# Kernel optimization log

Measured on AMD Instinct MI355X. Metric: run time of the kernel, lower is better.

Reference implementation:

```python
import jax, jax.numpy as jnp
from jax import lax
import numpy as np

# ----- static optical constants (from config) -----
N = 500            # phase mask grid
PX = 1e-6          # pixel pitch [m]
WL = 532e-9        # wavelength [m]
FL = 0.1           # focal length [m]
RI = 1.0           # refractive index
FWHC = 150e-6      # laser beam FWHC
K = 2.0 * np.pi * RI / WL
QE, DARK_MEAN, READ_STD, GAIN, MAX_ADU = 0.9, 0.005, 1.6, 2.0, 65535.0
MAX_VAL = 4.0e9    # Normalize01 max
PHOTONS = 1.0e6    # photons per emitter (max_intensity-style scaling)
R = 15             # psf_keep_radius -> 31x31 crops

_x = np.arange(-N // 2, N // 2) * PX
_X, _Y = np.meshgrid(_x, _x)
INCIDENT = np.exp(-(_X**2 + _Y**2) / (2.0 * FWHC**2)).astype(np.float32)
_C1 = (np.pi / (WL * FL) * (_X**2 + _Y**2)) % (2.0 * np.pi)
B1 = np.exp(-1j * _C1).astype(np.complex64)
# angular-spectrum gamma, directly in unshifted fft order
_F = np.fft.fftfreq(N, d=PX)
_A, _B = np.meshgrid(RI * WL * _F, RI * WL * _F)
GAMMA = np.sqrt(np.maximum(1.0 - _A**2 - _B**2, 0.0)).astype(np.float32)

def _gauss7():
    m = (7 - 1) / 2.0
    y, x = np.ogrid[-m:m + 1, -m:m + 1]
    h = np.exp(-(x * x + y * y) / 2.0)
    h[h < np.finfo(h.dtype).eps * h.max()] = 0
    return h.astype(np.float32)
GAUSS7 = _gauss7()


def setup_inputs() -> dict:
    key = jax.random.key(0)
    k1, k2, k3, k4, k5, k6, k7 = jax.random.split(key, 7)
    B, Ne = 8, 64
    phase_mask = jax.random.uniform(k1, (N, N), jnp.float32, 0.0, 2.0 * np.pi)
    zs = jax.random.uniform(k2, (Ne,), jnp.float32, 0.0, 1e-4)  # defocus depths [m]
    xyz = jax.random.randint(k3, (B, Ne, 2), 0, 170, jnp.int32) + 15  # in [15,184]
    std_u = jax.random.uniform(k4, (1,), jnp.float32)
    eps_dark = jax.random.normal(k5, (B, 1, 198, 198), jnp.float32)
    eps_photon = jax.random.normal(k6, (B, 1, 198, 198), jnp.float32)
    eps_read = jax.random.normal(k7, (B, 1, 198, 198), jnp.float32)
    return {"phase_mask": phase_mask, "zs": zs, "xyz": xyz, "std_u": std_u,
            "eps_dark": eps_dark, "eps_photon": eps_photon, "eps_read": eps_read}


def _forward(phase_mask, zs, xyz, std_u, eps_dark, eps_photon, eps_read):
    Bn, Ne = xyz.shape[0], xyz.shape[1]
    # --- FFT-based PSF generation (angular spectrum propagation) ---
    field = (INCIDENT * jnp.exp(1j * phase_mask) * B1).astype(jnp.complex64)  # [N,N]
    Ef = jnp.fft.fft2(field)                                                  # [N,N]
    H = jnp.exp(1j * ((K * GAMMA)[None] * zs[:, None, None]))                 # [Ne,N,N]
    Eprop = jnp.fft.ifft2(Ef[None] * H)                                       # [Ne,N,N]
    inten = jnp.abs(Eprop) ** 2
    c = N // 2
    psf = inten[:, c - R:c + R + 1, c - R:c + R + 1]                          # [Ne,31,31]
    psf = psf / (jnp.sum(psf, (-2, -1), keepdims=True) + 1e-12) * PHOTONS
    images4D = jnp.broadcast_to(psf[None], (Bn, Ne, 2 * R + 1, 2 * R + 1))
    # --- imgs4dto3d: scatter-add 31x31 patches into 200x200 canvas ---
    offs = jnp.arange(2 * R + 1) - R
    rows = xyz[..., 0][..., None, None] + offs[None, None, :, None]           # [B,Ne,31,1]
    cols = xyz[..., 1][..., None, None] + offs[None, None, None, :]           # [B,Ne,1,31]
    bidx = jnp.arange(Bn)[:, None, None, None]
    canvas = jnp.zeros((Bn, 200, 200), psf.dtype).at[bidx, rows, cols].add(images4D)
    img = canvas[:, None]                                                     # [B,1,200,200]
    # --- BlurLayer: per-draw std gaussian, conv pad=2 -> 198x198 ---
    std = 0.8 + 0.4 * std_u[0]
    s2 = std * std
    kern = (1.0 / (2.0 * jnp.pi * s2)) * GAUSS7 ** (1.0 / s2)
    blurred = lax.conv_general_dilated(img, kern[None, None], (1, 1),
                                       [(2, 2), (2, 2)],
                                       dimension_numbers=("NCHW", "OIHW", "NCHW"))
    # --- NoiseLayer (reparameterized gaussian approximations) ---
    sig = blurred * QE
    dark = DARK_MEAN + eps_dark * jnp.sqrt(jnp.float32(DARK_MEAN))
    total = jnp.maximum(sig + dark, 0.0)
    noisy = total + eps_photon * jnp.sqrt(jnp.maximum(total, 1e-12))
    elec = noisy + eps_read * READ_STD
    adu = jnp.clip(elec * GAIN, 0.0, MAX_ADU)
    # --- Normalize01 ---
    out = jnp.where(adu <= 10.0, 1.0, jnp.minimum(adu, MAX_VAL)) / MAX_VAL
    return out.astype(jnp.float32)


def reference(phase_mask, zs, xyz, std_u, eps_dark, eps_photon, eps_read):
    return _forward(phase_mask, zs, xyz, std_u, eps_dark, eps_photon, eps_read)
```

## Files before the change

### kernel.cpp

```cpp
#include <hip/hip_runtime.h>
#include <math.h>

#define NN 500
#define NE 64
#define BATCH 8
#define RR 15
#define PW 31
#define CAN 200
#define OHW 198
#define TWO_PI_F 6.28318530717958647692f
#define SETUP_N (BATCH * CAN * CAN + NE + 49)

#define BCH 16
#define BKC 64
#define BSTR 72
#define BG_CHUNK (2 * 64 * BSTR)
#define NLD (BG_CHUNK * 2 / 16)
#define ASCALE (1.0f / 64.0f)
#define PART_HALF_F ((size_t)NE * NN * 64)

using f16x8 = __attribute__((ext_vector_type(8))) _Float16;
using f32x4 = __attribute__((ext_vector_type(4))) float;

__device__ __forceinline__ void fast_sincos_red(float theta, float* s, float* c) {
    const float INV2PI = 0.15915494309189535f;
    const float PI2_HI = 6.28318548202514648f;
    const float PI2_LO = -1.7484556e-7f;
    float n = rintf(theta * INV2PI);
    float r = fmaf(n, -PI2_HI, theta);
    r = fmaf(n, -PI2_LO, r);
    *s = __sinf(r);
    *c = __cosf(r);
}

__global__ void k_setup(const float* __restrict__ std_u,
                        float* __restrict__ kgamma,
                        float2* __restrict__ tw,
                        float* __restrict__ kern,
                        float* __restrict__ canvas,
                        float* __restrict__ psf_sums) {
    int idx = blockIdx.x * blockDim.x + threadIdx.x;
    if (idx < NN) {
        double th = 2.0 * M_PI * (double)idx / (double)NN;
        tw[idx] = make_float2((float)cos(th), (float)sin(th));
    }
    if (idx < BATCH * CAN * CAN) canvas[idx] = 0.f;
    if (idx >= BATCH * CAN * CAN && idx < BATCH * CAN * CAN + NE)
        psf_sums[idx - BATCH * CAN * CAN] = 0.f;
    if (idx >= BATCH * CAN * CAN + NE && idx < SETUP_N) {
        int t = idx - (BATCH * CAN * CAN + NE);
        float stdv = 0.8f + 0.4f * std_u[0];
        float s2 = stdv * stdv;
        int a = t / 7 - 3, b = t % 7 - 3;
        float g = (float)exp(-0.5 * (double)(a * a + b * b));
        kern[t] = (1.0f / (2.0f * (float)M_PI * s2)) * powf(g, 1.0f / s2);
    }
    if (idx >= NN * NN) return;
    int i = idx / NN, j = idx % NN;
    double fy = (double)((i < 250) ? i : i - 500) * 2000.0;
    double fx = (double)((j < 250) ? j : j - 500) * 2000.0;
    double a = 5.32e-7 * fx;
    double b = 5.32e-7 * fy;
    double g = 1.0 - a * a - b * b;
    g = (g > 0.0) ? sqrt(g) : 0.0;
    float Kf = (float)(2.0 * M_PI * 1.0 / 5.32e-7);
    kgamma[idx] = Kf * (float)g;
}

__global__ void k_setup_b(_Float16* __restrict__ Bg) {
    int idx = blockIdx.x * blockDim.x + threadIdx.x;
    if (idx >= BCH * 64 * BSTR) return;
    int c = idx / (64 * BSTR);
    int rem = idx % (64 * BSTR);
    int nu = rem / BSTR, j = rem % BSTR;
    float hi = 0.f, lo = 0.f;
    int kap = c * BKC + j;
    if (j < BKC && kap < 2 * NN) {
        int u = kap >> 1, p = kap & 1;
        int ri = nu >> 1, q = nu & 1;
        int r = 235 + ri;
        int m = (u * r) % NN;
        double th = 2.0 * M_PI * (double)m / (double)NN;
        double wre = cos(th), wim = sin(th);
        double val = (q == 0) ? ((p == 0) ? wre : -wim)
                              : ((p == 0) ? wim : wre);
        float x = (float)val;
        _Float16 h = (_Float16)x;
        hi = (float)h;
        lo = x - (float)h;
    }
    size_t base = (size_t)c * BG_CHUNK + (size_t)nu * BSTR + j;
    Bg[base] = (_Float16)hi;
    Bg[base + (size_t)64 * BSTR] = (_Float16)lo;
}

__device__ __forceinline__ void ct_dft_stages(const float2* xs, const float2* tts,
                                              float2* S, int t,
                                              float2* out1, float2* out2, int* kout) {
    if (t < 250) {
        int d = t / 25;
        int b = t % 25;
        float2 st = tts[(25 * d) % NN];
        float wr = 1.f, wi = 0.f;
        float Er = 0.f, Ei = 0.f, Or_ = 0.f, Oi = 0.f;
#pragma unroll
        for (int a = 0; a < 20; a += 2) {
            float2 x0 = xs[25 * a + b];
            Er += x0.x * wr - x0.y * wi;
            Ei += x0.x * wi + x0.y * wr;
            float nr = wr * st.x - wi * st.y;
            float ni = wr * st.y + wi * st.x;
            float2 x1 = xs[25 * (a + 1) + b];
            Or_ += x1.x * nr - x1.y * ni;
            Oi  += x1.x * ni + x1.y * nr;
            wr = nr * st.x - ni * st.y;
            wi = nr * st.y + ni * st.x;
        }
        S[b * 21 + d]      = make_float2(Er + Or_, Ei + Oi);
        S[b * 21 + d + 10] = make_float2(Er - Or_, Ei - Oi);
    }
    __syncthreads();
    if (t < 250) {
        int k = t;
        int d1 = k % 20;
        int d2 = (d1 + 10) % 20;
        float2 s1 = tts[k];
        float wr = 1.f, wi = 0.f;
        float a1r = 0.f, a1i = 0.f, a2r = 0.f, a2i = 0.f;
#pragma unroll
        for (int b = 0; b < 25; ++b) {
            float2 u1 = S[b * 21 + d1];
            float2 u2 = S[b * 21 + d2];
            a1r += u1.x * wr - u1.y * wi;
            a1i += u1.x * wi + u1.y * wr;
            float sgnb = (b & 1) ? -1.f : 1.f;
            float w2r = sgnb * wr, w2i = sgnb * wi;
            a2r += u2.x * w2r - u2.y * w2i;
            a2i += u2.x * w2i + u2.y * w2r;
            float nr = wr * s1.x - wi * s1.y;
            wi = wr * s1.y + wi * s1.x;
            wr = nr;
        }
        *out1 = make_float2(a1r, a1i);
        *out2 = make_float2(a2r, a2i);
        *kout = k;
    }
}

__global__ void k_dft_rows(const float* __restrict__ phase, float2* __restrict__ dst,
                           const float2* __restrict__ tw) {
    __shared__ __align__(16) float2 xs[NN];
    __shared__ float2 tts[NN];
    __shared__ float2 S[25 * 21];
    int line = blockIdx.x;
    int t = threadIdx.x;
    const float INV2SIG = 2.2222222e7f;
    const float C1M = (float)(M_PI / 5.32e-8);
    float y = (float)(line - 250) * 1e-6f;
    float y2 = y * y;
    const float* prow = phase + (size_t)line * NN;
    for (int n = t; n < NN; n += 256) {
        float x = (float)(n - 250) * 1e-6f;
        float r2 = x * x + y2;
        float inc = __expf(-r2 * INV2SIG);
        float c1 = C1M * r2;
        float b1r = __cosf(c1), b1i = -__sinf(c1);
        float ph = prow[n];
        float sp = __sinf(ph), cp = __cosf(ph);
        float ar = inc * cp, ai = inc * sp;
        xs[n] = make_float2(ar * b1r - ai * b1i, ar * b1i + ai * b1r);
        float2 tt = tw[n];
        tts[n] = make_float2(tt.x, -tt.y);
    }
    __syncthreads();
    float2 o1, o2; int k;
    ct_dft_stages(xs, tts, S, t, &o1, &o2, &k);
    if (t < 250) {
        dst[(size_t)k * NN + line] = o1;
        dst[(size_t)(k + 250) * NN + line] = o2;
    }
}

__global__ void k_dft_cols(const float2* __restrict__ src, float2* __restrict__ dst,
                           const float2* __restrict__ tw) {
    __shared__ __align__(16) float2 xs[NN];
    __shared__ float2 tts[NN];
    __shared__ float2 S[25 * 21];
    int line = blockIdx.x;
    const float2* s = src + (size_t)line * NN;
    int t = threadIdx.x;
    for (int n = t; n < NN; n += 256) {
        xs[n] = s[n];
        float2 tt = tw[n];
        tts[n] = make_float2(tt.x, -tt.y);
    }
    __syncthreads();
    float2 o1, o2; int k;
    ct_dft_stages(xs, tts, S, t, &o1, &o2, &k);
    if (t < 250) {
        float2* dp = dst + (size_t)line * NN;
        dp[k] = o1;
        dp[k + 250] = o2;
    }
}

__global__ void __launch_bounds__(256, 4)
k_prop_mfma(const float2* __restrict__ EfT,
            const float* __restrict__ kgamma,
            const float* __restrict__ zs,
            const _Float16* __restrict__ Bg,
            float* __restrict__ part) {
    __shared__ __align__(16) _Float16 Bbuf[2][BG_CHUNK];
    __shared__ __align__(16) float2 eft[256];
    __shared__ __align__(16) float kgs[256];
    int v = blockIdx.x;
    int kh = blockIdx.y;
    int t = threadIdx.x;
    int w = t >> 6;
    int lane = t & 63;
    int lrow = lane & 15;
    int grp = lane >> 4;

    {
        int u = 256 * kh + t;
        if (u < NN) {
            eft[t] = EfT[(size_t)v * NN + u];
            kgs[t] = kgamma[(size_t)v * NN + u];
        } else {
            eft[t] = make_float2(0.f, 0.f);
            kgs[t] = 0.f;
        }
    }
    {
        const float4* srcb = (const float4*)(Bg + (size_t)(8 * kh) * BG_CHUNK);
        float4* dstb = (float4*)&Bbuf[0][0];
        for (int i = t; i < NLD; i += 256) dstb[i] = srcb[i];
    }
    float zv = zs[w * 16 + lrow];
    __syncthreads();

    f32x4 acc[4] = {};

#define MODSPLIT(ex, ey, kgv, i0) do {                                        \
        float s_, c_;                                                         \
        fast_sincos_red((kgv) * zv, &s_, &c_);                                \
        float yr = ((ex) * c_ - (ey) * s_) * ASCALE;                          \
        float yi = ((ex) * s_ + (ey) * c_) * ASCALE;                          \
        _Float16 h0 = (_Float16)yr;                                           \
        ah[i0] = h0; al[i0] = (_Float16)(yr - (float)h0);                     \
        _Float16 h1 = (_Float16)yi;                                           \
        ah[i0 + 1] = h1; al[i0 + 1] = (_Float16)(yi - (float)h1);             \
    } while (0)

    for (int ci = 0; ci < 8; ++ci) {
        float4 stg[5];
        if (ci + 1 < 8) {
            const float4* srcb =
                (const float4*)(Bg + (size_t)(8 * kh + ci + 1) * BG_CHUNK);
#pragma unroll
            for (int k = 0; k < 5; ++k) {
                int i = t + k * 256;
                if (i < NLD) stg[k] = srcb[i];
            }
        }
        const _Float16* Bb = &Bbuf[ci & 1][0];
#pragma unroll
        for (int sl = 0; sl < 2; ++sl) {
            int s_loc = ci * 2 + sl;
            int u0 = s_loc * 16 + grp * 4;
            f16x8 ah, al;
            {
                float4 e01 = *(const float4*)&eft[u0];
                float4 e23 = *(const float4*)&eft[u0 + 2];
                float4 kg4 = *(const float4*)&kgs[u0];
                MODSPLIT(e01.x, e01.y, kg4.x, 0);
                MODSPLIT(e01.z, e01.w, kg4.y, 2);
                MODSPLIT(e23.x, e23.y, kg4.z, 4);
                MODSPLIT(e23.z, e23.w, kg4.w, 6);
            }
            int koff = sl * 32 + grp * 8;
#pragma unroll
            for (int nt = 0; nt < 4; ++nt) {
                int nu = nt * 16 + lrow;
                f16x8 bh = *(const f16x8*)&Bb[nu * BSTR + koff];
                f16x8 bl = *(const f16x8*)&Bb[64 * BSTR + nu * BSTR + koff];
                acc[nt] = __builtin_amdgcn_mfma_f32_16x16x32_f16(ah, bh, acc[nt], 0, 0, 0);
                acc[nt] = __builtin_amdgcn_mfma_f32_16x16x32_f16(al, bh, acc[nt], 0, 0, 0);
                acc[nt] = __builtin_amdgcn_mfma_f32_16x16x32_f16(ah, bl, acc[nt], 0, 0, 0);
            }
        }
        if (ci + 1 < 8) {
            float4* dstb = (float4*)&Bbuf[(ci + 1) & 1][0];
#pragma unroll
            for (int k = 0; k < 5; ++k) {
                int i = t + k * 256;
                if (i < NLD) dstb[i] = stg[k];
            }
        }
        __syncthreads();
    }
#undef MODSPLIT

    float* pf = part + (size_t)kh * PART_HALF_F;
#pragma unroll
    for (int nt = 0; nt < 4; ++nt) {
        int nu = nt * 16 + lrow;
#pragma unroll
        for (int rg = 0; rg < 4; ++rg) {
            int z = w * 16 + grp * 4 + rg;
            pf[((size_t)z * NN + v) * 64 + nu] = acc[nt][rg];
        }
    }
}

__global__ void k_prop_cols(const float* __restrict__ part,
                            float* __restrict__ psf,
                            float* __restrict__ psf_sums) {
    __shared__ __align__(16) float X2[NN][16];
    int rq = blockIdx.x;
    int z  = blockIdx.y;
    int t  = threadIdx.x;
    const float* p0 = part + ((size_t)z * NN) * 64 + rq * 16;
    const float* p1 = p0 + PART_HALF_F;
    for (int i = t; i < NN * 4; i += 256) {
        int v = i >> 2, q4 = i & 3;
        float4 a = *(const float4*)(p0 + (size_t)v * 64 + q4 * 4);
        float4 b = *(const float4*)(p1 + (size_t)v * 64 + q4 * 4);
        *(float4*)&X2[v][q4 * 4] =
            make_float4(a.x + b.x, a.y + b.y, a.z + b.z, a.w + b.w);
    }
    __syncthreads();
    int ril = t >> 5;
    int ri  = rq * 8 + ril;
    int ci  = t & 31;
    float val = 0.f;
    if (ri < PW && ci < PW) {
        int c = 235 + ci;
        float ar = 0.f, ai = 0.f;
        float sr, si;
        {
            float th = (TWO_PI_F / NN) * (float)(c % NN);
            sincosf(th, &si, &sr);
        }
        for (int vb = 0; vb < 4; ++vb) {
            int v0 = vb * 125;
            float wr, wi;
            float th = (TWO_PI_F / NN) * (float)((v0 * c) % NN);
            sincosf(th, &wi, &wr);
            for (int v = v0; v < v0 + 125; ++v) {
                float2 xy = *(const float2*)&X2[v][2 * ril];
                ar += xy.x * wr - xy.y * wi;
                ai += xy.x * wi + xy.y * wr;
                float nwr = wr * sr - wi * si;
                wi = wr * si + wi * sr;
                wr = nwr;
            }
        }
        const float inv = 64.0f / 250000.0f;
        float re = ar * inv, im = ai * inv;
        val = re * re + im * im;
        psf[(size_t)z * (PW * PW) + ri * PW + ci] = val;
    }
#pragma unroll
    for (int m = 1; m < 64; m <<= 1) val += __shfl_xor(val, m);
    if ((t & 63) == 0) atomicAdd(&psf_sums[z], val);
}

__global__ void k_scatter(const float* __restrict__ psf,
                          const float* __restrict__ psf_sums,
                          const int* __restrict__ xyz,
                          float* __restrict__ canvas) {
    int e = blockIdx.x;
    int b = blockIdx.y;
    int r0 = xyz[(b * NE + e) * 2 + 0] - RR;
    int c0 = xyz[(b * NE + e) * 2 + 1] - RR;
    float sc = 1.0e6f / (psf_sums[e] + 1e-12f);
    float* cb = canvas + (size_t)b * (CAN * CAN);
    for (int p = threadIdx.x; p < PW * PW; p += blockDim.x) {
        int i = p / PW, j = p % PW;
        atomicAdd(cb + (r0 + i) * CAN + (c0 + j), psf[e * PW * PW + p] * sc);
    }
}

__global__ void k_final(const float* __restrict__ canvas,
                        const float* __restrict__ kern,
                        const float* __restrict__ eps_dark,
                        const float* __restrict__ eps_photon,
                        const float* __restrict__ eps_read,
                        float* __restrict__ out) {
    __shared__ float kk[49];
    __shared__ float tile[14][40];
    int b = blockIdx.z;
    int tx = threadIdx.x, ty = threadIdx.y;
    int t = ty * 32 + tx;
    int j0 = blockIdx.x * 32, i0 = blockIdx.y * 8;
    if (t < 49) kk[t] = kern[t];
    const float* cb = canvas + (size_t)b * (CAN * CAN);
    for (int p = t; p < 14 * 38; p += 256) {
        int rr = p / 38, cc = p % 38;
        int gi = i0 + rr - 2, gj = j0 + cc - 2;
        tile[rr][cc] = (gi >= 0 && gi < CAN && gj >= 0 && gj < CAN)
                           ? cb[gi * CAN + gj] : 0.f;
    }
    __syncthreads();
    int i = i0 + ty, j = j0 + tx;
    if (i >= OHW || j >= OHW) return;
    float acc = 0.f;
#pragma unroll
    for (int a = 0; a < 7; ++a)
#pragma unroll
        for (int q = 0; q < 7; ++q)
            acc += tile[ty + a][tx + q] * kk[a * 7 + q];
    int idx = b * (OHW * OHW) + i * OHW + j;
    float sig = acc * 0.9f;
    float dark = 0.005f + eps_dark[idx] * sqrtf(0.005f);
    float total = fmaxf(sig + dark, 0.0f);
    float noisy = total + eps_photon[idx] * sqrtf(fmaxf(total, 1e-12f));
    float elec = noisy + eps_read[idx] * 1.6f;
    float adu = fminf(fmaxf(elec * 2.0f, 0.0f), 65535.0f);
    float v = (adu <= 10.0f) ? 1.0f : fminf(adu, 4.0e9f);
    out[idx] = v / 4.0e9f;
}

extern "C" void kernel_launch(void* const* d_in, const int* in_sizes, int n_in,
                              void* d_out, int out_size, void* d_ws, size_t ws_size,
                              hipStream_t stream) {
    const float* phase    = (const float*)d_in[0];
    const float* zs       = (const float*)d_in[1];
    const int*   xyz      = (const int*)d_in[2];
    const float* std_u    = (const float*)d_in[3];
    const float* epsd     = (const float*)d_in[4];
    const float* epsp     = (const float*)d_in[5];
    const float* epsr     = (const float*)d_in[6];
    float* out = (float*)d_out;

    char* ws = (char*)d_ws;
    size_t off = 0;
    auto alloc = [&](size_t bytes) {
        off = (off + 255) & ~(size_t)255;
        size_t o = off; off += bytes; return o;
    };
    float*  kgamma   = (float*) (ws + alloc((size_t)NN * NN * 4));
    float2* tw       = (float2*)(ws + alloc((size_t)NN * 8));
    float2* R1T      = (float2*)(ws + alloc((size_t)NN * NN * 8));
    float2* EfT      = (float2*)(ws + alloc((size_t)NN * NN * 8));
    float*  part     = (float*) (ws + alloc(2 * PART_HALF_F * 4));
    float*  psf      = (float*) (ws + alloc((size_t)NE * PW * PW * 4));
    float*  psf_sums = (float*) (ws + alloc((size_t)NE * 4));
    float*  kern     = (float*) (ws + alloc((size_t)64 * 4));
    float*  canvas   = (float*) (ws + alloc((size_t)BATCH * CAN * CAN * 4));
    _Float16* Bg     = (_Float16*)(ws + alloc((size_t)BCH * BG_CHUNK * 2));
    (void)ws_size; (void)n_in; (void)in_sizes; (void)out_size;

    k_setup<<<(SETUP_N + 255) / 256, 256, 0, stream>>>(
        std_u, kgamma, tw, kern, canvas, psf_sums);
    k_setup_b<<<(BCH * 64 * BSTR + 255) / 256, 256, 0, stream>>>(Bg);
    k_dft_rows<<<NN, 256, 0, stream>>>(phase, R1T, tw);
    k_dft_cols<<<NN, 256, 0, stream>>>(R1T, EfT, tw);
    k_prop_mfma<<<dim3(NN, 2), 256, 0, stream>>>(EfT, kgamma, zs, Bg, part);
    k_prop_cols<<<dim3(4, NE), 256, 0, stream>>>(part, psf, psf_sums);
    k_scatter<<<dim3(NE, BATCH), 256, 0, stream>>>(psf, psf_sums, xyz, canvas);
    k_final<<<dim3((OHW + 31) / 32, (OHW + 7) / 8, BATCH), dim3(32, 8), 0, stream>>>(
        canvas, kern, epsd, epsp, epsr, out);
}
```

Measured before the change: 160.6 us.

## Switch propagation GEMM to 32x32 MFMA with in-block K-split reduction

The two-block K-split of the propagation GEMM is merged into one block per column. The four waves are split into two K-halves by two z-halves, each using 32x32x16 MFMA tiles, and the two halves are reduced through shared memory before a single coalesced float4 store. This removes the second partial buffer, so the column kernel no longer adds two halves. The B-matrix setup kernel is also folded into k_setup, saving one launch. In exchange the grid is halved to 500 blocks, each block does twice the work with less pipelining (a single B buffer plus an extra barrier per chunk), and the launch bound drops occupancy to 3.

Result: slower. 164.2 us (+2.2%).

```diff
diff --git a/kernel.cpp b/kernel.cpp
--- a/kernel.cpp
+++ b/kernel.cpp
@@ -15,12 +15,10 @@
 #define BKC 64
 #define BSTR 72
 #define BG_CHUNK (2 * 64 * BSTR)
-#define NLD (BG_CHUNK * 2 / 16)
 #define ASCALE (1.0f / 64.0f)
-#define PART_HALF_F ((size_t)NE * NN * 64)
 
 using f16x8 = __attribute__((ext_vector_type(8))) _Float16;
-using f32x4 = __attribute__((ext_vector_type(4))) float;
+using f32x16 = __attribute__((ext_vector_type(16))) float;
 
 __device__ __forceinline__ void fast_sincos_red(float theta, float* s, float* c) {
     const float INV2PI = 0.15915494309189535f;
@@ -38,11 +36,36 @@
                         float2* __restrict__ tw,
                         float* __restrict__ kern,
                         float* __restrict__ canvas,
-                        float* __restrict__ psf_sums) {
+                        float* __restrict__ psf_sums,
+                        _Float16* __restrict__ Bg) {
     int idx = blockIdx.x * blockDim.x + threadIdx.x;
     if (idx < NN) {
         double th = 2.0 * M_PI * (double)idx / (double)NN;
         tw[idx] = make_float2((float)cos(th), (float)sin(th));
+    }
+    if (idx < BCH * 64 * BSTR) {
+        int c = idx / (64 * BSTR);
+        int rem = idx % (64 * BSTR);
+        int nu = rem / BSTR, j = rem % BSTR;
+        float hi = 0.f, lo = 0.f;
+        int kap = c * BKC + j;
+        if (j < BKC && kap < 2 * NN) {
+            int u = kap >> 1, p = kap & 1;
+            int ri = nu >> 1, q = nu & 1;
+            int r = 235 + ri;
+            int m = (u * r) % NN;
+            double th = 2.0 * M_PI * (double)m / (double)NN;
+            double wre = cos(th), wim = sin(th);
+            double val = (q == 0) ? ((p == 0) ? wre : -wim)
+                                  : ((p == 0) ? wim : wre);
+            float x = (float)val;
+            _Float16 h = (_Float16)x;
+            hi = (float)h;
+            lo = x - (float)h;
+        }
+        size_t base = (size_t)c * BG_CHUNK + (size_t)nu * BSTR + j;
+        Bg[base] = (_Float16)hi;
+        Bg[base + (size_t)64 * BSTR] = (_Float16)lo;
     }
     if (idx < BATCH * CAN * CAN) canvas[idx] = 0.f;
     if (idx >= BATCH * CAN * CAN && idx < BATCH * CAN * CAN + NE)
@@ -65,33 +88,6 @@
     g = (g > 0.0) ? sqrt(g) : 0.0;
     float Kf = (float)(2.0 * M_PI * 1.0 / 5.32e-7);
     kgamma[idx] = Kf * (float)g;
-}
-
-__global__ void k_setup_b(_Float16* __restrict__ Bg) {
-    int idx = blockIdx.x * blockDim.x + threadIdx.x;
-    if (idx >= BCH * 64 * BSTR) return;
-    int c = idx / (64 * BSTR);
-    int rem = idx % (64 * BSTR);
-    int nu = rem / BSTR, j = rem % BSTR;
-    float hi = 0.f, lo = 0.f;
-    int kap = c * BKC + j;
-    if (j < BKC && kap < 2 * NN) {
-        int u = kap >> 1, p = kap & 1;
-        int ri = nu >> 1, q = nu & 1;
-        int r = 235 + ri;
-        int m = (u * r) % NN;
-        double th = 2.0 * M_PI * (double)m / (double)NN;
-        double wre = cos(th), wim = sin(th);
-        double val = (q == 0) ? ((p == 0) ? wre : -wim)
-                              : ((p == 0) ? wim : wre);
-        float x = (float)val;
-        _Float16 h = (_Float16)x;
-        hi = (float)h;
-        lo = x - (float)h;
-    }
-    size_t base = (size_t)c * BG_CHUNK + (size_t)nu * BSTR + j;
-    Bg[base] = (_Float16)hi;
-    Bg[base + (size_t)64 * BSTR] = (_Float16)lo;
 }
 
 __device__ __forceinline__ void ct_dft_stages(const float2* xs, const float2* tts,
@@ -204,70 +200,77 @@
     }
 }
 
-__global__ void __launch_bounds__(256, 4)
+__global__ void __launch_bounds__(256, 3)
 k_prop_mfma(const float2* __restrict__ EfT,
             const float* __restrict__ kgamma,
             const float* __restrict__ zs,
             const _Float16* __restrict__ Bg,
             float* __restrict__ part) {
-    __shared__ __align__(16) _Float16 Bbuf[2][BG_CHUNK];
-    __shared__ __align__(16) float2 eft[256];
-    __shared__ __align__(16) float kgs[256];
+    __shared__ __align__(16) char smem[2 * BG_CHUNK * 2 + 512 * 8 + 512 * 4];
+    _Float16* Bbuf = (_Float16*)smem;
+    float2*   eft  = (float2*)(smem + 2 * BG_CHUNK * 2);
+    float*    kgs  = (float*)(smem + 2 * BG_CHUNK * 2 + 512 * 8);
+    float*    ctile = (float*)smem;
+
     int v = blockIdx.x;
-    int kh = blockIdx.y;
     int t = threadIdx.x;
     int w = t >> 6;
+    int wh = w >> 1;
+    int mw = w & 1;
     int lane = t & 63;
-    int lrow = lane & 15;
-    int grp = lane >> 4;
-
+    int l31 = lane & 31;
+    int lk = lane >> 5;
+
+    for (int n = t; n < 512; n += 256) {
+        if (n < NN) {
+            float2 e = EfT[(size_t)v * NN + n];
+            eft[n] = make_float2(e.x * ASCALE, e.y * ASCALE);
+            kgs[n] = kgamma[(size_t)v * NN + n];
+        } else {
+            eft[n] = make_float2(0.f, 0.f);
+            kgs[n] = 0.f;
+        }
+    }
     {
-        int u = 256 * kh + t;
-        if (u < NN) {
-            eft[t] = EfT[(size_t)v * NN + u];
-            kgs[t] = kgamma[(size_t)v * NN + u];
-        } else {
-            eft[t] = make_float2(0.f, 0.f);
-            kgs[t] = 0.f;
-        }
-    }
-    {
-        const float4* srcb = (const float4*)(Bg + (size_t)(8 * kh) * BG_CHUNK);
-        float4* dstb = (float4*)&Bbuf[0][0];
-        for (int i = t; i < NLD; i += 256) dstb[i] = srcb[i];
-    }
-    float zv = zs[w * 16 + lrow];
-    __syncthreads();
-
-    f32x4 acc[4] = {};
+        for (int k = 0; k < 9; ++k) {
+            int i = t + k * 256;
+            int whs = i / 1152, off = i % 1152;
+            ((float4*)Bbuf)[i] =
+                ((const float4*)(Bg + (size_t)(8 * whs) * BG_CHUNK))[off];
+        }
+    }
+    float zv = zs[mw * 32 + l31];
+    __syncthreads();
+
+    f32x16 acc[2] = {};
 
 #define MODSPLIT(ex, ey, kgv, i0) do {                                        \
         float s_, c_;                                                         \
         fast_sincos_red((kgv) * zv, &s_, &c_);                                \
-        float yr = ((ex) * c_ - (ey) * s_) * ASCALE;                          \
-        float yi = ((ex) * s_ + (ey) * c_) * ASCALE;                          \
+        float yr = (ex) * c_ - (ey) * s_;                                     \
+        float yi = (ex) * s_ + (ey) * c_;                                     \
         _Float16 h0 = (_Float16)yr;                                           \
         ah[i0] = h0; al[i0] = (_Float16)(yr - (float)h0);                     \
         _Float16 h1 = (_Float16)yi;                                           \
         ah[i0 + 1] = h1; al[i0 + 1] = (_Float16)(yi - (float)h1);             \
     } while (0)
 
+    const _Float16* Bb = Bbuf + wh * BG_CHUNK;
     for (int ci = 0; ci < 8; ++ci) {
-        float4 stg[5];
+        float4 stg[9];
         if (ci + 1 < 8) {
-            const float4* srcb =
-                (const float4*)(Bg + (size_t)(8 * kh + ci + 1) * BG_CHUNK);
-#pragma unroll
-            for (int k = 0; k < 5; ++k) {
+#pragma unroll
+            for (int k = 0; k < 9; ++k) {
                 int i = t + k * 256;
-                if (i < NLD) stg[k] = srcb[i];
-            }
-        }
-        const _Float16* Bb = &Bbuf[ci & 1][0];
-#pragma unroll
-        for (int sl = 0; sl < 2; ++sl) {
-            int s_loc = ci * 2 + sl;
-            int u0 = s_loc * 16 + grp * 4;
+                int whs = i / 1152, off = i % 1152;
+                stg[k] = ((const float4*)(Bg +
+                            (size_t)(8 * whs + ci + 1) * BG_CHUNK))[off];
+            }
+        }
+#pragma unroll
+        for (int sl = 0; sl < 4; ++sl) {
+            int step = ci * 4 + sl;
+            int u0 = wh * 256 + step * 8 + lk * 4;
             f16x8 ah, al;
             {
                 float4 e01 = *(const float4*)&eft[u0];
@@ -278,38 +281,55 @@
                 MODSPLIT(e23.x, e23.y, kg4.z, 4);
                 MODSPLIT(e23.z, e23.w, kg4.w, 6);
             }
-            int koff = sl * 32 + grp * 8;
-#pragma unroll
-            for (int nt = 0; nt < 4; ++nt) {
-                int nu = nt * 16 + lrow;
+            int koff = sl * 16 + lk * 8;
+#pragma unroll
+            for (int nt = 0; nt < 2; ++nt) {
+                int nu = nt * 32 + l31;
                 f16x8 bh = *(const f16x8*)&Bb[nu * BSTR + koff];
                 f16x8 bl = *(const f16x8*)&Bb[64 * BSTR + nu * BSTR + koff];
-                acc[nt] = __builtin_amdgcn_mfma_f32_16x16x32_f16(ah, bh, acc[nt], 0, 0, 0);
-                acc[nt] = __builtin_amdgcn_mfma_f32_16x16x32_f16(al, bh, acc[nt], 0, 0, 0);
-                acc[nt] = __builtin_amdgcn_mfma_f32_16x16x32_f16(ah, bl, acc[nt], 0, 0, 0);
-            }
-        }
+                acc[nt] = __builtin_amdgcn_mfma_f32_32x32x16_f16(ah, bh, acc[nt], 0, 0, 0);
+                acc[nt] = __builtin_amdgcn_mfma_f32_32x32x16_f16(al, bh, acc[nt], 0, 0, 0);
+                acc[nt] = __builtin_amdgcn_mfma_f32_32x32x16_f16(ah, bl, acc[nt], 0, 0, 0);
+            }
+        }
+        __syncthreads();
         if (ci + 1 < 8) {
-            float4* dstb = (float4*)&Bbuf[(ci + 1) & 1][0];
-#pragma unroll
-            for (int k = 0; k < 5; ++k) {
+#pragma unroll
+            for (int k = 0; k < 9; ++k) {
                 int i = t + k * 256;
-                if (i < NLD) dstb[i] = stg[k];
+                ((float4*)Bbuf)[i] = stg[k];
             }
         }
         __syncthreads();
     }
 #undef MODSPLIT
 
-    float* pf = part + (size_t)kh * PART_HALF_F;
-#pragma unroll
-    for (int nt = 0; nt < 4; ++nt) {
-        int nu = nt * 16 + lrow;
-#pragma unroll
-        for (int rg = 0; rg < 4; ++rg) {
-            int z = w * 16 + grp * 4 + rg;
-            pf[((size_t)z * NN + v) * 64 + nu] = acc[nt][rg];
-        }
+    if (wh == 0) {
+#pragma unroll
+        for (int nt = 0; nt < 2; ++nt)
+#pragma unroll
+            for (int reg = 0; reg < 16; ++reg) {
+                int row = (reg & 3) + 8 * (reg >> 2) + 4 * lk;
+                ctile[(mw * 32 + row) * 64 + nt * 32 + l31] = acc[nt][reg];
+            }
+    }
+    __syncthreads();
+    if (wh == 1) {
+#pragma unroll
+        for (int nt = 0; nt < 2; ++nt)
+#pragma unroll
+            for (int reg = 0; reg < 16; ++reg) {
+                int row = (reg & 3) + 8 * (reg >> 2) + 4 * lk;
+                ctile[(mw * 32 + row) * 64 + nt * 32 + l31] += acc[nt][reg];
+            }
+    }
+    __syncthreads();
+#pragma unroll
+    for (int p = 0; p < 4; ++p) {
+        int idx = p * 256 + t;
+        int z = idx >> 4, c4 = idx & 15;
+        float4 val = *(const float4*)&ctile[z * 64 + c4 * 4];
+        *(float4*)&part[((size_t)z * NN + v) * 64 + c4 * 4] = val;
     }
 }
 
@@ -321,13 +341,10 @@
     int z  = blockIdx.y;
     int t  = threadIdx.x;
     const float* p0 = part + ((size_t)z * NN) * 64 + rq * 16;
-    const float* p1 = p0 + PART_HALF_F;
     for (int i = t; i < NN * 4; i += 256) {
         int v = i >> 2, q4 = i & 3;
         float4 a = *(const float4*)(p0 + (size_t)v * 64 + q4 * 4);
-        float4 b = *(const float4*)(p1 + (size_t)v * 64 + q4 * 4);
-        *(float4*)&X2[v][q4 * 4] =
-            make_float4(a.x + b.x, a.y + b.y, a.z + b.z, a.w + b.w);
+        *(float4*)&X2[v][q4 * 4] = a;
     }
     __syncthreads();
     int ril = t >> 5;
@@ -444,7 +461,7 @@
     float2* tw       = (float2*)(ws + alloc((size_t)NN * 8));
     float2* R1T      = (float2*)(ws + alloc((size_t)NN * NN * 8));
     float2* EfT      = (float2*)(ws + alloc((size_t)NN * NN * 8));
-    float*  part     = (float*) (ws + alloc(2 * PART_HALF_F * 4));
+    float*  part     = (float*) (ws + alloc((size_t)NE * NN * 64 * 4));
     float*  psf      = (float*) (ws + alloc((size_t)NE * PW * PW * 4));
     float*  psf_sums = (float*) (ws + alloc((size_t)NE * 4));
     float*  kern     = (float*) (ws + alloc((size_t)64 * 4));
@@ -453,11 +470,10 @@
     (void)ws_size; (void)n_in; (void)in_sizes; (void)out_size;
 
     k_setup<<<(SETUP_N + 255) / 256, 256, 0, stream>>>(
-        std_u, kgamma, tw, kern, canvas, psf_sums);
-    k_setup_b<<<(BCH * 64 * BSTR + 255) / 256, 256, 0, stream>>>(Bg);
+        std_u, kgamma, tw, kern, canvas, psf_sums, Bg);
     k_dft_rows<<<NN, 256, 0, stream>>>(phase, R1T, tw);
     k_dft_cols<<<NN, 256, 0, stream>>>(R1T, EfT, tw);
-    k_prop_mfma<<<dim3(NN, 2), 256, 0, stream>>>(EfT, kgamma, zs, Bg, part);
+    k_prop_mfma<<<NN, 256, 0, stream>>>(EfT, kgamma, zs, Bg, part);
     k_prop_cols<<<dim3(4, NE), 256, 0, stream>>>(part, psf, psf_sums);
     k_scatter<<<dim3(NE, BATCH), 256, 0, stream>>>(psf, psf_sums, xyz, canvas);
     k_final<<<dim3((OHW + 31) / 32, (OHW + 7) / 8, BATCH), dim3(32, 8), 0, stream>>>(
```
